# Kernel optimization log

Hardware: AMD Instinct MI355X
Metric: run time of the kernel (lower is better)

## Reference

```python
import jax, jax.numpy as jnp
import numpy as np

IN_DIM = 256
QK_DIM = IN_DIM // 8


def setup_inputs() -> dict:
    key = jax.random.key(0)
    ks = jax.random.split(key, 10)
    B, C, W, H = 4, IN_DIM, 64, 64
    a = jax.random.normal(ks[0], (B, C, W, H), dtype=jnp.float32)
    b = jax.random.normal(ks[1], (B, C, W, H), dtype=jnp.float32)
    c = jax.random.uniform(ks[2], (B, 1, 2 * W, 2 * H), dtype=jnp.float32)
    scale = 0.02
    wq = jax.random.normal(ks[3], (QK_DIM, C), dtype=jnp.float32) * scale
    bq = jnp.zeros((QK_DIM,), dtype=jnp.float32)
    wk = jax.random.normal(ks[4], (QK_DIM, C), dtype=jnp.float32) * scale
    bk = jnp.zeros((QK_DIM,), dtype=jnp.float32)
    wv = jax.random.normal(ks[5], (C, C), dtype=jnp.float32) * scale
    bv = jnp.zeros((C,), dtype=jnp.float32)
    gamma = jnp.ones((1,), dtype=jnp.float32)
    return {"a": a, "b": b, "c": c, "wq": wq, "bq": bq, "wk": wk,
            "bk": bk, "wv": wv, "bv": bv, "gamma": gamma}


def reference(a, b, c, wq, bq, wk, bk, wv, bv, gamma):
    B, C, W, H = a.shape
    N = W * H
    # F.interpolate(c, scale_factor=1/down_rate, mode='nearest'): output idx i -> input idx i*down_rate
    down = c.shape[2] // W
    cd = c[:, :, ::down, ::down]                      # [B,1,W,H]
    # 1x1 convs as channel contractions
    q = jnp.einsum('bchw,oc->bohw', a, wq) + bq[None, :, None, None]
    k = jnp.einsum('bchw,oc->bohw', b, wk) + bk[None, :, None, None]
    v = jnp.einsum('bchw,oc->bohw', a, wv) + bv[None, :, None, None]
    qf = q.reshape(B, QK_DIM, N)                      # proj_query^T rows are spatial
    kf = k.reshape(B, QK_DIM, N)
    vf = v.reshape(B, C, N)
    sim = jnp.einsum('bdi,bdj->bij', qf, kf)          # [B,N,N]
    cflat = cd.reshape(B, N)
    # mask[b,i,j] = cflat[b,i] (per-query multiplicative logit scaling)
    logits = sim * cflat[:, :, None]
    attn = jax.nn.softmax(logits, axis=-1)            # [B,N,N]
    out_attn = jnp.einsum('bcj,bij->bci', vf, attn).reshape(B, C, W, H)
    out = gamma * a * cd + (1.0 - cd) * out_attn
    return out
```

## Files before the change

### kernel.cpp

```cpp
#include <hip/hip_runtime.h>

#define LOG2E 1.44269504088896340736f

typedef __attribute__((ext_vector_type(8))) short short8;
typedef __attribute__((ext_vector_type(4))) float float4v;
typedef __attribute__((ext_vector_type(2))) float float2v;
typedef __attribute__((ext_vector_type(2))) int int2v;

__device__ inline unsigned short f2bf(float f) {
    union { float f; unsigned u; } v; v.f = f;
    unsigned r = v.u + 0x7fffu + ((v.u >> 16) & 1u);
    return (unsigned short)(r >> 16);
}
__device__ inline float bf2f(unsigned short u) {
    union { unsigned u; float f; } v; v.u = ((unsigned)u) << 16;
    return v.f;
}
__device__ inline unsigned pk_bf16(float a, float b) {
    union { float f; unsigned u; } ua, ub; ua.f = a; ub.f = b;
    return __builtin_amdgcn_perm(ub.u + 0x8000u, ua.u + 0x8000u, 0x07060302u);
}

__global__ void wcvt_kernel(const float* __restrict__ wq, const float* __restrict__ wk,
                            const float* __restrict__ wv, unsigned short* __restrict__ Wbf)
{
    int idx = blockIdx.x * 256 + threadIdx.x;
    int e4  = idx * 4;
    int row = e4 >> 8, col = e4 & 255;
    const float* src = (row < 32) ? (wq + row * 256 + col)
                     : (row < 64) ? (wk + (row - 32) * 256 + col)
                                  : (wv + (row - 64) * 256 + col);
    float4v v = *(const float4v*)src;
    int2v p;
    p.x = (unsigned)f2bf(v[0]) | ((unsigned)f2bf(v[1]) << 16);
    p.y = (unsigned)f2bf(v[2]) | ((unsigned)f2bf(v[3]) << 16);
    *(int2v*)(Wbf + e4) = p;
}

__launch_bounds__(256, 3)
__global__ void proj_kernel(const float* __restrict__ a_p, const float* __restrict__ b_p,
                            const float* __restrict__ c_p,
                            const float* __restrict__ bq, const float* __restrict__ bk,
                            const float* __restrict__ bv,
                            const unsigned short* __restrict__ Wbf,
                            unsigned short* __restrict__ Qg, unsigned short* __restrict__ Kg,
                            unsigned short* __restrict__ Vg)
{
    __shared__ unsigned At[16 * 132];
    __shared__ unsigned Bt[16 * 132];

    const int t    = threadIdx.x;
    const int blk  = blockIdx.x;
    const int b    = blk & 3;
    const int t16  = blk >> 2;
    const int i0   = t16 * 16;
    const int lane = t & 63;
    const int w    = t >> 6;
    const int q    = lane >> 4;
    const int n    = lane & 15;

    {
        int arr = t >> 7, p = t & 127;
        const float* src = (arr ? b_p : a_p) + ((size_t)(b * 256 + 2 * p)) * 4096 + i0;
        unsigned* dst = (arr ? Bt : At) + p;
#pragma unroll
        for (int h = 0; h < 2; ++h) {
            float4v r0a = *(const float4v*)(src + h * 8);
            float4v r0b = *(const float4v*)(src + h * 8 + 4);
            float4v r1a = *(const float4v*)(src + 4096 + h * 8);
            float4v r1b = *(const float4v*)(src + 4096 + h * 8 + 4);
#pragma unroll
            for (int jj = 0; jj < 4; ++jj)
                dst[(h * 8 + jj) * 132] = (unsigned)f2bf(r0a[jj]) | ((unsigned)f2bf(r1a[jj]) << 16);
#pragma unroll
            for (int jj = 0; jj < 4; ++jj)
                dst[(h * 8 + 4 + jj) * 132] = (unsigned)f2bf(r0b[jj]) | ((unsigned)f2bf(r1b[jj]) << 16);
        }
    }
    __syncthreads();

    float4v acc[5];
#pragma unroll
    for (int kk = 0; kk < 5; ++kk) acc[kk] = (float4v){0.f, 0.f, 0.f, 0.f};

#pragma unroll 2
    for (int kc = 0; kc < 8; ++kc) {
        short8 atf = *(const short8*)((const unsigned short*)At + n * 264 + kc * 32 + q * 8);
        short8 btf = atf;
        if (w >= 2)
            btf = *(const short8*)((const unsigned short*)Bt + n * 264 + kc * 32 + q * 8);
#pragma unroll
        for (int kk = 0; kk < 5; ++kk) {
            int mt = w + 4 * kk;
            short8 wf = *(const short8*)(Wbf + (size_t)(mt * 16 + n) * 256 + kc * 32 + q * 8);
            short8 bsel = (mt == 2 || mt == 3) ? btf : atf;
            acc[kk] = __builtin_amdgcn_mfma_f32_16x16x32_bf16(wf, bsel, acc[kk], 0, 0, 0);
        }
    }

    const int i = i0 + n;
    const int jj = i & 31;
    const int pperm = ((jj & 15) >> 2) * 8 + (jj >> 4) * 4 + (jj & 3);
    const float cdq = c_p[b * 16384 + (i >> 6) * 256 + (i & 63) * 2] * LOG2E;
#pragma unroll
    for (int kk = 0; kk < 5; ++kk) {
        int mt = w + 4 * kk;
#pragma unroll
        for (int r = 0; r < 4; ++r) {
            int mm = mt * 16 + q * 4 + r;
            float bias = (mm < 32) ? bq[mm] : (mm < 64) ? bk[mm - 32] : bv[mm - 64];
            float val = acc[kk][r] + bias;
            if (mm < 32) {
                Qg[(size_t)(b * 4096 + i) * 32 + mm] = f2bf(val * cdq);
            } else if (mm < 64) {
                Kg[(size_t)(b * 4096 + i) * 32 + (mm - 32)] = f2bf(val);
            } else {
                Vg[(size_t)(((b * 128 + (i >> 5)) * 256) + (mm - 64)) * 32 + pperm] = f2bf(val);
            }
        }
    }
}

__launch_bounds__(256, 3)
__global__ void attn_kernel(const unsigned short* __restrict__ Qg,
                            const unsigned short* __restrict__ Kg,
                            const unsigned short* __restrict__ Vg,
                            unsigned short* __restrict__ Opart, float* __restrict__ lsum)
{
    const int t    = threadIdx.x;
    const int blk  = blockIdx.x;
    const int b    = blk & 3;
    const int s_lo = (blk >> 2) & 1;
    const int rt   = (blk >> 3) & 63;
    const int s    = s_lo + 2 * (blk >> 9);
    const int lidx = (s << 8) | (rt << 2) | b;
    const int i0   = rt * 64;
    const int lane = t & 63;
    const int w    = t >> 6;
    const int q    = lane >> 4;
    const int n    = lane & 15;

    short8 qf[4];
#pragma unroll
    for (int ig = 0; ig < 4; ++ig)
        qf[ig] = *(const short8*)(Qg + (size_t)(b * 4096 + i0 + ig * 16 + n) * 32 + q * 8);

    float4v acc[4][4];
#pragma unroll
    for (int ig = 0; ig < 4; ++ig)
#pragma unroll
        for (int ct = 0; ct < 4; ++ct) acc[ig][ct] = (float4v){0.f, 0.f, 0.f, 0.f};
    float lsc[4] = {0.f, 0.f, 0.f, 0.f};

    const float4v m16v = (float4v){-16.f, -16.f, -16.f, -16.f};

    const unsigned short* kb = Kg + (size_t)(b * 4096 + s * 1024 + n) * 32 + q * 8;
    const unsigned short* vb = Vg + ((size_t)((b * 128 + s * 32) * 256 + w * 64 + n)) * 32 + q * 8;

    short8 kf0 = *(const short8*)(kb);
    short8 kf1 = *(const short8*)(kb + 512);

#pragma unroll 1
    for (int it = 0; it < 32; ++it) {
        short8 vf[4];
#pragma unroll
        for (int ct = 0; ct < 4; ++ct)
            vf[ct] = *(const short8*)(vb + ct * 512);

        short8 pf[4];
#pragma unroll
        for (int ig = 0; ig < 4; ++ig) {
            float4v s0 = __builtin_amdgcn_mfma_f32_16x16x32_bf16(kf0, qf[ig], m16v, 0, 0, 0);
            float4v s1 = __builtin_amdgcn_mfma_f32_16x16x32_bf16(kf1, qf[ig], m16v, 0, 0, 0);
            float p0 = __builtin_amdgcn_exp2f(s0[0]), p1 = __builtin_amdgcn_exp2f(s0[1]);
            float p2 = __builtin_amdgcn_exp2f(s0[2]), p3 = __builtin_amdgcn_exp2f(s0[3]);
            float p4 = __builtin_amdgcn_exp2f(s1[0]), p5 = __builtin_amdgcn_exp2f(s1[1]);
            float p6 = __builtin_amdgcn_exp2f(s1[2]), p7 = __builtin_amdgcn_exp2f(s1[3]);
            lsc[ig] += ((p0 + p1) + (p2 + p3)) + ((p4 + p5) + (p6 + p7));
            union { short8 s8; unsigned u[4]; } pf_;
            pf_.u[0] = pk_bf16(p0, p1);
            pf_.u[1] = pk_bf16(p2, p3);
            pf_.u[2] = pk_bf16(p4, p5);
            pf_.u[3] = pk_bf16(p6, p7);
            pf[ig] = pf_.s8;
        }

        kf0 = *(const short8*)(kb + 1024);
        kf1 = *(const short8*)(kb + 1536);

#pragma unroll
        for (int ig = 0; ig < 4; ++ig)
#pragma unroll
            for (int ct = 0; ct < 4; ++ct)
                acc[ig][ct] = __builtin_amdgcn_mfma_f32_16x16x32_bf16(pf[ig], vf[ct], acc[ig][ct], 0, 0, 0);

        kb += 1024;
        vb += 8192;
    }

    const size_t obase = (size_t)lidx * 16384;
#pragma unroll
    for (int ig = 0; ig < 4; ++ig)
#pragma unroll
        for (int ct = 0; ct < 4; ++ct) {
            int c = w * 64 + ct * 16 + n;
            int i = ig * 16 + q * 4;
            unsigned long long pk =
                (unsigned long long)pk_bf16(acc[ig][ct][0], acc[ig][ct][1]) |
                ((unsigned long long)pk_bf16(acc[ig][ct][2], acc[ig][ct][3]) << 32);
            __builtin_nontemporal_store(pk,
                (unsigned long long*)(Opart + obase + (size_t)c * 64 + i));
        }
#pragma unroll
    for (int ig = 0; ig < 4; ++ig) {
        float v = lsc[ig];
        v += __shfl_xor(v, 16, 64);
        v += __shfl_xor(v, 32, 64);
        if (w == 0 && lane < 16)
            lsum[(size_t)lidx * 64 + ig * 16 + lane] = v;
    }
}

__launch_bounds__(256, 4)
__global__ void combine_kernel(const float* __restrict__ a_p, const float* __restrict__ c_p,
                               const float* __restrict__ gamma_p,
                               const unsigned short* __restrict__ Opart,
                               const float* __restrict__ lsum, float* __restrict__ out)
{
    __shared__ float invL[64];
    __shared__ float cdl[64];

    const int t   = threadIdx.x;
    const int blk = blockIdx.x;
    const int b   = blk & 3;
    const int rt  = (blk >> 2) & 63;
    const int cs  = blk >> 8;
    const int i0  = rt * 64;

    if (t < 64) {
        float L = 0.f;
#pragma unroll
        for (int s = 0; s < 4; ++s)
            L += lsum[(size_t)((s << 8) | (rt << 2) | b) * 64 + t];
        invL[t] = 1.0f / L;
        cdl[t] = c_p[b * 16384 + rt * 256 + 2 * t];
    }
    __syncthreads();

    const float gam = gamma_p[0];
    const int il = (t & 31) * 2;
    const int cq = t >> 5;
#pragma unroll
    for (int k = 0; k < 4; ++k) {
        int c = cs * 32 + cq + 8 * k;
        float o0 = 0.f, o1 = 0.f;
#pragma unroll
        for (int s = 0; s < 4; ++s) {
            int idx = (s << 8) | (rt << 2) | b;
            unsigned pr = *(const unsigned*)(Opart + (size_t)idx * 16384 + (size_t)c * 64 + il);
            o0 += bf2f((unsigned short)(pr & 0xffff));
            o1 += bf2f((unsigned short)(pr >> 16));
        }
        o0 *= invL[il];
        o1 *= invL[il + 1];
        size_t gi = (size_t)(b * 256 + c) * 4096 + i0 + il;
        float2v av = *(const float2v*)(a_p + gi);
        float cd0 = cdl[il], cd1 = cdl[il + 1];
        float2v ov;
        ov[0] = gam * av[0] * cd0 + (1.0f - cd0) * o0;
        ov[1] = gam * av[1] * cd1 + (1.0f - cd1) * o1;
        *(float2v*)(out + gi) = ov;
    }
}

extern "C" void kernel_launch(void* const* d_in, const int* in_sizes, int n_in,
                              void* d_out, int out_size, void* d_ws, size_t ws_size,
                              hipStream_t stream)
{
    const float* a_p   = (const float*)d_in[0];
    const float* b_p   = (const float*)d_in[1];
    const float* c_p   = (const float*)d_in[2];
    const float* wq    = (const float*)d_in[3];
    const float* bq    = (const float*)d_in[4];
    const float* wk    = (const float*)d_in[5];
    const float* bk    = (const float*)d_in[6];
    const float* wv    = (const float*)d_in[7];
    const float* bv    = (const float*)d_in[8];
    const float* gamma = (const float*)d_in[9];
    float* out = (float*)d_out;

    unsigned short* Qg    = (unsigned short*)d_ws;
    unsigned short* Kg    = Qg + (size_t)4 * 4096 * 32;
    unsigned short* Vg    = Kg + (size_t)4 * 4096 * 32;
    unsigned short* Wbf   = Vg + (size_t)4 * 256 * 4096;
    unsigned short* Opart = Wbf + (size_t)320 * 256;
    float*          lsum  = (float*)(Opart + (size_t)1024 * 16384);

    wcvt_kernel<<<80, 256, 0, stream>>>(wq, wk, wv, Wbf);
    proj_kernel<<<1024, 256, 0, stream>>>(a_p, b_p, c_p, bq, bk, bv, Wbf, Qg, Kg, Vg);
    attn_kernel<<<1024, 256, 0, stream>>>(Qg, Kg, Vg, Opart, lsum);
    combine_kernel<<<2048, 256, 0, stream>>>(a_p, c_p, gamma, Opart, lsum, out);
}
```

Before: 197.2 us.

## Enlarge projection tiles to 64 pixels and stage outputs through LDS

The projection kernel now handles 64 spatial positions per 512-thread block instead of 16 per 256-thread block. Each weight fragment loaded from global memory is therefore reused across four pixel subtiles. Q, K and V results are first written to shared memory and then stored to global memory with 16-byte coalesced writes, replacing scattered 2-byte stores, and bias and mask values are cached in LDS. The attention output store also switches from a nontemporal 64-bit store to a plain vector store. The risks are fewer blocks (256) with higher register and LDS pressure, plus extra barriers.

Measured after the change: 188.5 us. 1.05x faster.

```diff
diff --git a/kernel.cpp b/kernel.cpp
--- a/kernel.cpp
+++ b/kernel.cpp
@@ -6,6 +6,7 @@
 typedef __attribute__((ext_vector_type(4))) float float4v;
 typedef __attribute__((ext_vector_type(2))) float float2v;
 typedef __attribute__((ext_vector_type(2))) int int2v;
+typedef __attribute__((ext_vector_type(4))) int int4v;
 
 __device__ inline unsigned short f2bf(float f) {
     union { float f; unsigned u; } v; v.f = f;
@@ -37,7 +38,7 @@
     *(int2v*)(Wbf + e4) = p;
 }
 
-__launch_bounds__(256, 3)
+__launch_bounds__(512, 2)
 __global__ void proj_kernel(const float* __restrict__ a_p, const float* __restrict__ b_p,
                             const float* __restrict__ c_p,
                             const float* __restrict__ bq, const float* __restrict__ bk,
@@ -46,77 +47,110 @@
                             unsigned short* __restrict__ Qg, unsigned short* __restrict__ Kg,
                             unsigned short* __restrict__ Vg)
 {
-    __shared__ unsigned At[16 * 132];
-    __shared__ unsigned Bt[16 * 132];
+    __shared__ __align__(16) unsigned short At[64 * 264];
+    __shared__ __align__(16) unsigned short Bt[64 * 264];
+    __shared__ float bias[320];
+    __shared__ float cdl[64];
 
     const int t    = threadIdx.x;
     const int blk  = blockIdx.x;
     const int b    = blk & 3;
-    const int t16  = blk >> 2;
-    const int i0   = t16 * 16;
+    const int tile = blk >> 2;
+    const int i0   = tile * 64;
     const int lane = t & 63;
     const int w    = t >> 6;
     const int q    = lane >> 4;
     const int n    = lane & 15;
+    const int it   = w & 3;
+    const int mh   = w >> 2;
 
     {
-        int arr = t >> 7, p = t & 127;
-        const float* src = (arr ? b_p : a_p) + ((size_t)(b * 256 + 2 * p)) * 4096 + i0;
-        unsigned* dst = (arr ? Bt : At) + p;
-#pragma unroll
-        for (int h = 0; h < 2; ++h) {
+        const int arr = t >> 8, cp = (t >> 1) & 127, ih = (t & 1) * 32;
+        const float* src = (arr ? b_p : a_p) + ((size_t)(b * 256 + 2 * cp)) * 4096 + i0 + ih;
+        unsigned* dst = (unsigned*)(arr ? Bt : At) + cp;
+#pragma unroll
+        for (int h = 0; h < 4; ++h) {
             float4v r0a = *(const float4v*)(src + h * 8);
             float4v r0b = *(const float4v*)(src + h * 8 + 4);
             float4v r1a = *(const float4v*)(src + 4096 + h * 8);
             float4v r1b = *(const float4v*)(src + 4096 + h * 8 + 4);
 #pragma unroll
             for (int jj = 0; jj < 4; ++jj)
-                dst[(h * 8 + jj) * 132] = (unsigned)f2bf(r0a[jj]) | ((unsigned)f2bf(r1a[jj]) << 16);
+                dst[(ih + h * 8 + jj) * 132] = pk_bf16(r0a[jj], r1a[jj]);
 #pragma unroll
             for (int jj = 0; jj < 4; ++jj)
-                dst[(h * 8 + 4 + jj) * 132] = (unsigned)f2bf(r0b[jj]) | ((unsigned)f2bf(r1b[jj]) << 16);
-        }
+                dst[(ih + h * 8 + 4 + jj) * 132] = pk_bf16(r0b[jj], r1b[jj]);
+        }
+        if (t < 320) bias[t] = (t < 32) ? bq[t] : (t < 64) ? bk[t - 32] : bv[t - 64];
+        else if (t < 384) cdl[t - 320] = c_p[b * 16384 + tile * 256 + (t - 320) * 2];
     }
     __syncthreads();
 
-    float4v acc[5];
-#pragma unroll
-    for (int kk = 0; kk < 5; ++kk) acc[kk] = (float4v){0.f, 0.f, 0.f, 0.f};
+    float4v acc[10];
+#pragma unroll
+    for (int j = 0; j < 10; ++j) acc[j] = (float4v){0.f, 0.f, 0.f, 0.f};
 
 #pragma unroll 2
     for (int kc = 0; kc < 8; ++kc) {
-        short8 atf = *(const short8*)((const unsigned short*)At + n * 264 + kc * 32 + q * 8);
-        short8 btf = atf;
-        if (w >= 2)
-            btf = *(const short8*)((const unsigned short*)Bt + n * 264 + kc * 32 + q * 8);
-#pragma unroll
-        for (int kk = 0; kk < 5; ++kk) {
-            int mt = w + 4 * kk;
+        short8 xa = *(const short8*)&At[(it * 16 + n) * 264 + kc * 32 + q * 8];
+        short8 xb = xa;
+        if (mh == 0)
+            xb = *(const short8*)&Bt[(it * 16 + n) * 264 + kc * 32 + q * 8];
+#pragma unroll
+        for (int j = 0; j < 10; ++j) {
+            int mt = mh * 10 + j;
             short8 wf = *(const short8*)(Wbf + (size_t)(mt * 16 + n) * 256 + kc * 32 + q * 8);
-            short8 bsel = (mt == 2 || mt == 3) ? btf : atf;
-            acc[kk] = __builtin_amdgcn_mfma_f32_16x16x32_bf16(wf, bsel, acc[kk], 0, 0, 0);
-        }
-    }
-
-    const int i = i0 + n;
-    const int jj = i & 31;
-    const int pperm = ((jj & 15) >> 2) * 8 + (jj >> 4) * 4 + (jj & 3);
-    const float cdq = c_p[b * 16384 + (i >> 6) * 256 + (i & 63) * 2] * LOG2E;
-#pragma unroll
-    for (int kk = 0; kk < 5; ++kk) {
-        int mt = w + 4 * kk;
-#pragma unroll
-        for (int r = 0; r < 4; ++r) {
-            int mm = mt * 16 + q * 4 + r;
-            float bias = (mm < 32) ? bq[mm] : (mm < 64) ? bk[mm - 32] : bv[mm - 64];
-            float val = acc[kk][r] + bias;
-            if (mm < 32) {
-                Qg[(size_t)(b * 4096 + i) * 32 + mm] = f2bf(val * cdq);
-            } else if (mm < 64) {
-                Kg[(size_t)(b * 4096 + i) * 32 + (mm - 32)] = f2bf(val);
+            short8 bsel = (mt == 2 || mt == 3) ? xb : xa;
+            acc[j] = __builtin_amdgcn_mfma_f32_16x16x32_bf16(wf, bsel, acc[j], 0, 0, 0);
+        }
+    }
+    __syncthreads();
+
+    unsigned short* QKst = At;
+    unsigned short* Vst  = Bt;
+    {
+        const float cdq = cdl[it * 16 + n] * LOG2E;
+#pragma unroll
+        for (int j = 0; j < 10; ++j) {
+            int mt = mh * 10 + j;
+            float4v bv4 = *(const float4v*)&bias[mt * 16 + q * 4];
+            float v0 = acc[j][0] + bv4[0], v1 = acc[j][1] + bv4[1];
+            float v2 = acc[j][2] + bv4[2], v3 = acc[j][3] + bv4[3];
+            if (mt < 2) {
+                v0 *= cdq; v1 *= cdq; v2 *= cdq; v3 *= cdq;
+                int2v pk; pk.x = (int)pk_bf16(v0, v1); pk.y = (int)pk_bf16(v2, v3);
+                *(int2v*)&QKst[(it * 16 + n) * 72 + mt * 16 + q * 4] = pk;
+            } else if (mt < 4) {
+                int2v pk; pk.x = (int)pk_bf16(v0, v1); pk.y = (int)pk_bf16(v2, v3);
+                *(int2v*)&QKst[(it * 16 + n) * 72 + mt * 16 + q * 4] = pk;
             } else {
-                Vg[(size_t)(((b * 128 + (i >> 5)) * 256) + (mm - 64)) * 32 + pperm] = f2bf(val);
+                int p = ((n >> 2) * 8) + ((it & 1) * 4) + (n & 3);
+                int cbase = mt * 16 - 64 + q * 4;
+                int jb = it >> 1;
+                Vst[((jb * 256) + cbase + 0) * 32 + p] = f2bf(v0);
+                Vst[((jb * 256) + cbase + 1) * 32 + p] = f2bf(v1);
+                Vst[((jb * 256) + cbase + 2) * 32 + p] = f2bf(v2);
+                Vst[((jb * 256) + cbase + 3) * 32 + p] = f2bf(v3);
             }
+        }
+    }
+    __syncthreads();
+
+    {
+        int i = t >> 3, h8 = t & 7;
+        int4v v = *(const int4v*)&QKst[i * 72 + h8 * 8];
+        unsigned short* dstp = (h8 < 4)
+            ? Qg + (size_t)(b * 4096 + i0 + i) * 32 + h8 * 8
+            : Kg + (size_t)(b * 4096 + i0 + i) * 32 + (h8 - 4) * 8;
+        *(int4v*)dstp = v;
+    }
+    {
+#pragma unroll
+        for (int k = 0; k < 4; ++k) {
+            int flat = k * 512 + t;
+            int4v v = *(const int4v*)&Vst[flat * 8];
+            int jb = flat >> 10;
+            *(int4v*)(Vg + (size_t)(b * 128 + tile * 2 + jb) * 8192 + (flat & 1023) * 8) = v;
         }
     }
 }
@@ -205,11 +239,10 @@
         for (int ct = 0; ct < 4; ++ct) {
             int c = w * 64 + ct * 16 + n;
             int i = ig * 16 + q * 4;
-            unsigned long long pk =
-                (unsigned long long)pk_bf16(acc[ig][ct][0], acc[ig][ct][1]) |
-                ((unsigned long long)pk_bf16(acc[ig][ct][2], acc[ig][ct][3]) << 32);
-            __builtin_nontemporal_store(pk,
-                (unsigned long long*)(Opart + obase + (size_t)c * 64 + i));
+            int2v pk;
+            pk.x = (int)pk_bf16(acc[ig][ct][0], acc[ig][ct][1]);
+            pk.y = (int)pk_bf16(acc[ig][ct][2], acc[ig][ct][3]);
+            *(int2v*)(Opart + obase + (size_t)c * 64 + i) = pk;
         }
 #pragma unroll
     for (int ig = 0; ig < 4; ++ig) {
@@ -297,7 +330,7 @@
     float*          lsum  = (float*)(Opart + (size_t)1024 * 16384);
 
     wcvt_kernel<<<80, 256, 0, stream>>>(wq, wk, wv, Wbf);
-    proj_kernel<<<1024, 256, 0, stream>>>(a_p, b_p, c_p, bq, bk, bv, Wbf, Qg, Kg, Vg);
+    proj_kernel<<<256, 512, 0, stream>>>(a_p, b_p, c_p, bq, bk, bv, Wbf, Qg, Kg, Vg);
     attn_kernel<<<1024, 256, 0, stream>>>(Qg, Kg, Vg, Opart, lsum);
     combine_kernel<<<2048, 256, 0, stream>>>(a_p, c_p, gamma, Opart, lsum, out);
 }
```
